# Kernel optimization log

Hardware: AMD Instinct MI355X
Metric: run time of the kernel (lower is better)

Reference implementation:

```python
import jax, jax.numpy as jnp
import numpy as np

def setup_inputs() -> dict:
    key = jax.random.key(0)
    k1, k2, k3, k4, k5 = jax.random.split(key, 5)
    B, Lc, Lq, D = 32, 512, 64, 1024
    return {
        "c": jax.random.normal(k1, (B, Lc, D), dtype=jnp.float32),
        "q": jax.random.normal(k2, (B, Lq, D), dtype=jnp.float32),
        "proj_c": jax.random.normal(k3, (D, 1), dtype=jnp.float32) * 0.04,
        "proj_q": jax.random.normal(k4, (D, 1), dtype=jnp.float32) * 0.04,
        "proj_cq": jax.random.normal(k5, (1, 1, D), dtype=jnp.float32) * 0.04,
    }

def reference(c, q, proj_c, proj_q, proj_cq):
    # similarity: s0 + s1 + s2, shape [B, Lc, Lq]
    s0 = c @ proj_c                                   # [B, Lc, 1]
    s1 = jnp.swapaxes(q @ proj_q, 1, 2)               # [B, 1, Lq]
    s2 = jnp.einsum('bcd,bqd->bcq', c * proj_cq, q)   # [B, Lc, Lq]
    sim = s0 + s1 + s2

    # context-to-query attention
    a_c2q = jax.nn.softmax(sim, axis=-1)              # [B, Lc, Lq]
    c2q = jnp.einsum('bcq,bqd->bcd', a_c2q, q)        # [B, Lc, D]

    # query-to-context attention (max over query dim, softmax over context)
    a_q2c = jax.nn.softmax(jnp.max(sim, axis=-1), axis=-1)  # [B, Lc]
    q2c = jnp.einsum('bc,bcd->bd', a_q2c, c)[:, None, :]    # [B, 1, D], broadcasts over Lc

    out = jnp.concatenate((c, c2q, c * q2c, c * c2q), axis=-1)  # [B, Lc, 4D]
    return out
```

## Files before the change

### kernel.cpp

```cpp
#include <hip/hip_runtime.h>

#define B 32
#define LC 512
#define LQ 64
#define DD 1024


typedef __attribute__((ext_vector_type(8))) short bf16x8;
typedef __attribute__((ext_vector_type(4))) float f32x4;

__device__ inline short f2bf(float f) {
    unsigned u = __builtin_bit_cast(unsigned, f);
    u += 0x7FFFu + ((u >> 16) & 1u);
    return (short)(u >> 16);
}

__device__ inline bf16x8 pack8(float4 a, float4 b) {
    bf16x8 r;
    r[0] = f2bf(a.x); r[1] = f2bf(a.y); r[2] = f2bf(a.z); r[3] = f2bf(a.w);
    r[4] = f2bf(b.x); r[5] = f2bf(b.y); r[6] = f2bf(b.z); r[7] = f2bf(b.w);
    return r;
}

__device__ inline float dot4(float4 a, float4 b) {
    return a.x * b.x + a.y * b.y + a.z * b.z + a.w * b.w;
}

__device__ inline int xswz(int bid, int nwg) {
    return (bid & 7) * (nwg >> 3) + (bid >> 3);
}

__device__ inline void xpose44(float v[4], int l15) {
    const bool m0 = l15 & 1, m1 = l15 & 2;
    float x0 = m0 ? v[0] : v[1];
    float x1 = m0 ? v[2] : v[3];
    x0 = __shfl_xor(x0, 1, 64);
    x1 = __shfl_xor(x1, 1, 64);
    if (m0) { v[0] = x0; v[2] = x1; } else { v[1] = x0; v[3] = x1; }
    float y0 = m1 ? v[0] : v[2];
    float y1 = m1 ? v[1] : v[3];
    y0 = __shfl_xor(y0, 2, 64);
    y1 = __shfl_xor(y1, 2, 64);
    if (m1) { v[0] = y0; v[1] = y1; } else { v[2] = y0; v[3] = y1; }
}

__global__ __launch_bounds__(256) void k0_q(const float* __restrict__ q,
                                            const float* __restrict__ proj_q,
                                            short* __restrict__ qbf,
                                            short* __restrict__ qT,
                                            float* __restrict__ s1part) {
    const int bid = xswz(blockIdx.x, 512);
    const int b  = bid >> 4;
    const int d0 = (bid & 15) * 64;
    const int sl = bid & 15;
    const int t  = threadIdx.x;

    __shared__ __align__(16) short tile[64][72];
    __shared__ float s1red[64][8];

    const int j0 = (t & 31) * 2;
    const int dg = t >> 5;

    const float* qr0 = q + (size_t)(b * LQ + j0) * DD + d0 + dg * 8;
    const float* qr1 = qr0 + DD;
    float4 x0 = *(const float4*)(qr0 + 0);
    float4 x1 = *(const float4*)(qr0 + 4);
    float4 y0 = *(const float4*)(qr1 + 0);
    float4 y1 = *(const float4*)(qr1 + 4);
    float4 p0 = *(const float4*)(proj_q + d0 + dg * 8);
    float4 p1 = *(const float4*)(proj_q + d0 + dg * 8 + 4);

    s1red[j0][dg]     = dot4(x0, p0) + dot4(x1, p1);
    s1red[j0 + 1][dg] = dot4(y0, p0) + dot4(y1, p1);

    *(bf16x8*)&qbf[(size_t)(b * LQ + j0) * DD + d0 + dg * 8]     = pack8(x0, x1);
    *(bf16x8*)&qbf[(size_t)(b * LQ + j0 + 1) * DD + d0 + dg * 8] = pack8(y0, y1);

    const float* fx0 = (const float*)&x0;
    const float* fx1 = (const float*)&x1;
    const float* fy0 = (const float*)&y0;
    const float* fy1 = (const float*)&y1;
#pragma unroll
    for (int e = 0; e < 8; ++e) {
        float v0 = (e < 4) ? fx0[e] : fx1[e - 4];
        float v1 = (e < 4) ? fy0[e] : fy1[e - 4];
        unsigned pk = (unsigned)(unsigned short)f2bf(v0)
                    | ((unsigned)(unsigned short)f2bf(v1) << 16);
        *(unsigned*)&tile[dg * 8 + e][j0] = pk;
    }
    __syncthreads();

    {
        const int d = t >> 2, part = t & 3;
        bf16x8 v0 = *(const bf16x8*)&tile[d][part * 16];
        bf16x8 v1 = *(const bf16x8*)&tile[d][part * 16 + 8];
        short* dst = qT + ((size_t)b * DD + d0 + d) * LQ + part * 16;
        *(bf16x8*)(dst)     = v0;
        *(bf16x8*)(dst + 8) = v1;
    }
    if (t < 64) {
        float s = 0.f;
#pragma unroll
        for (int k = 0; k < 8; ++k) s += s1red[t][k];
        s1part[(b * 16 + sl) * 64 + t] = s;
    }
}

__global__ __launch_bounds__(256) void k1_sim(const float* __restrict__ c,
                                              const short* __restrict__ qbf,
                                              const float* __restrict__ proj_c,
                                              const float* __restrict__ proj_cq,
                                              const float* __restrict__ s1part,
                                              short* __restrict__ P,
                                              float* __restrict__ mfull) {
    const int bid = xswz(blockIdx.x, 512);
    const int b  = bid >> 4;
    const int i0 = (bid & 15) * 32;
    const int t  = threadIdx.x;
    const int w  = t >> 6, lane = t & 63;
    const int l15 = lane & 15, quad = lane >> 4;

    __shared__ __align__(16) short sA[2][32][72];
    __shared__ float rmaxL[32][4];
    __shared__ float rsumL[32][4];
    __shared__ float s0red[32][8];
    __shared__ float s1L[64];

    const int arow = t >> 3, ag = t & 7;

    const float* cbase = c + (size_t)(b * LC + i0 + arow) * DD + ag * 8;
    const short* qfrag = qbf + (size_t)(b * LQ + w * 16 + l15) * DD + quad * 8;

    f32x4 acc[2] = {{0.f,0.f,0.f,0.f},{0.f,0.f,0.f,0.f}};
    float s0p = 0.f;

    float4 a0 = *(const float4*)(cbase + 0);
    float4 a1 = *(const float4*)(cbase + 4);
    bf16x8 bcur[2], bnxt[2];
#pragma unroll
    for (int s = 0; s < 2; ++s)
        bcur[s] = *(const bf16x8*)(qfrag + s * 32);
    {
        float4 p0 = *(const float4*)(proj_cq + ag * 8);
        float4 p1 = *(const float4*)(proj_cq + ag * 8 + 4);
        float4 c0 = *(const float4*)(proj_c + ag * 8);
        float4 c1 = *(const float4*)(proj_c + ag * 8 + 4);
        s0p += dot4(a0, c0) + dot4(a1, c1);
        float4 m0 = {a0.x * p0.x, a0.y * p0.y, a0.z * p0.z, a0.w * p0.w};
        float4 m1 = {a1.x * p1.x, a1.y * p1.y, a1.z * p1.z, a1.w * p1.w};
        *(bf16x8*)&sA[0][arow][ag * 8] = pack8(m0, m1);
    }
    a0 = *(const float4*)(cbase + 64);
    a1 = *(const float4*)(cbase + 68);
    __syncthreads();

    for (int kc = 0; kc < 16; ++kc) {
        const int cur = kc & 1;
        float4 na0, na1;
        if (kc < 14) {
            na0 = *(const float4*)(cbase + (kc + 2) * 64);
            na1 = *(const float4*)(cbase + (kc + 2) * 64 + 4);
        }
        if (kc < 15) {
#pragma unroll
            for (int s = 0; s < 2; ++s)
                bnxt[s] = *(const bf16x8*)(qfrag + (kc + 1) * 64 + s * 32);
        }
#pragma unroll
        for (int s = 0; s < 2; ++s) {
            int ko = s * 32 + quad * 8;
#pragma unroll
            for (int mt = 0; mt < 2; ++mt) {
                bf16x8 af = *(const bf16x8*)&sA[cur][mt * 16 + l15][ko];
                acc[mt] = __builtin_amdgcn_mfma_f32_16x16x32_bf16(af, bcur[s], acc[mt], 0, 0, 0);
            }
        }
        if (kc < 15) {
            const float* pcq = proj_cq + (kc + 1) * 64 + ag * 8;
            const float* pc  = proj_c  + (kc + 1) * 64 + ag * 8;
            float4 p0 = *(const float4*)(pcq + 0);
            float4 p1 = *(const float4*)(pcq + 4);
            float4 c0 = *(const float4*)(pc + 0);
            float4 c1 = *(const float4*)(pc + 4);
            s0p += dot4(a0, c0) + dot4(a1, c1);
            float4 m0 = {a0.x * p0.x, a0.y * p0.y, a0.z * p0.z, a0.w * p0.w};
            float4 m1 = {a1.x * p1.x, a1.y * p1.y, a1.z * p1.z, a1.w * p1.w};
            *(bf16x8*)&sA[cur ^ 1][arow][ag * 8] = pack8(m0, m1);
            a0 = na0; a1 = na1;
            bcur[0] = bnxt[0]; bcur[1] = bnxt[1];
        }
        __syncthreads();
    }

    s0red[arow][ag] = s0p;
    if (t < 64) {
        float s = 0.f;
#pragma unroll
        for (int k = 0; k < 16; ++k) s += s1part[(b * 16 + k) * 64 + t];
        s1L[t] = s;
    }
    __syncthreads();

    const float s1j = s1L[w * 16 + l15];
    float v[2][4];
#pragma unroll
    for (int mt = 0; mt < 2; ++mt) {
#pragma unroll
        for (int r = 0; r < 4; ++r) {
            float vv = acc[mt][r] + s1j;
            v[mt][r] = vv;
            float rm = vv;
#pragma unroll
            for (int off = 1; off < 16; off <<= 1) rm = fmaxf(rm, __shfl_xor(rm, off, 16));
            if (l15 == 0) rmaxL[mt * 16 + quad * 4 + r][w] = rm;
        }
    }
    __syncthreads();
    float e[2][4];
#pragma unroll
    for (int mt = 0; mt < 2; ++mt) {
#pragma unroll
        for (int r = 0; r < 4; ++r) {
            int row = mt * 16 + quad * 4 + r;
            float m = fmaxf(fmaxf(rmaxL[row][0], rmaxL[row][1]),
                            fmaxf(rmaxL[row][2], rmaxL[row][3]));
            float ee = __expf(v[mt][r] - m);
            e[mt][r] = ee;
            float se = ee;
#pragma unroll
            for (int off = 1; off < 16; off <<= 1) se += __shfl_xor(se, off, 16);
            if (l15 == 0) rsumL[row][w] = se;
        }
    }
    __syncthreads();
#pragma unroll
    for (int mt = 0; mt < 2; ++mt) {
#pragma unroll
        for (int r = 0; r < 4; ++r) {
            int row = mt * 16 + quad * 4 + r;
            float s = rsumL[row][0] + rsumL[row][1] + rsumL[row][2] + rsumL[row][3];
            P[(size_t)(b * LC + i0 + row) * LQ + w * 16 + l15] = f2bf(e[mt][r] / s);
        }
    }
    if (t < 32) {
        float s0v = 0.f;
#pragma unroll
        for (int k = 0; k < 8; ++k) s0v += s0red[t][k];
        float mm = fmaxf(fmaxf(rmaxL[t][0], rmaxL[t][1]),
                         fmaxf(rmaxL[t][2], rmaxL[t][3]));
        mfull[b * LC + i0 + t] = mm + s0v;
    }
}

__global__ __launch_bounds__(256) void k2_q2c(const float* __restrict__ c,
                                              const float* __restrict__ mfull,
                                              float* __restrict__ q2c) {
    const int bid = xswz(blockIdx.x, 256);
    const int b  = bid >> 3;
    const int d0 = (bid & 7) * 128;
    const int t  = threadIdx.x;
    __shared__ float aL[LC];
    __shared__ float redm[4];
    __shared__ float reds[4];

    float m0 = mfull[b * LC + t];
    float m1 = mfull[b * LC + 256 + t];
    float mx = fmaxf(m0, m1);
#pragma unroll
    for (int off = 32; off; off >>= 1) mx = fmaxf(mx, __shfl_xor(mx, off, 64));
    if ((t & 63) == 0) redm[t >> 6] = mx;
    __syncthreads();
    float bm = fmaxf(fmaxf(redm[0], redm[1]), fmaxf(redm[2], redm[3]));
    float e0 = __expf(m0 - bm), e1 = __expf(m1 - bm);
    float s = e0 + e1;
#pragma unroll
    for (int off = 32; off; off >>= 1) s += __shfl_xor(s, off, 64);
    if ((t & 63) == 0) reds[t >> 6] = s;
    __syncthreads();
    float bs = reds[0] + reds[1] + reds[2] + reds[3];
    float inv = 1.0f / bs;
    aL[t] = e0 * inv;
    aL[t + 256] = e1 * inv;
    __syncthreads();

    const int tx = t & 31, ty = t >> 5;
    float4 acc = {0.f, 0.f, 0.f, 0.f};
    const float* cb = c + (size_t)b * LC * DD + d0 + tx * 4;
    for (int i = ty; i < LC; i += 8) {
        float a = aL[i];
        float4 cv = *(const float4*)(cb + (size_t)i * DD);
        acc.x += a * cv.x; acc.y += a * cv.y; acc.z += a * cv.z; acc.w += a * cv.w;
    }
    __shared__ __align__(16) float4 red[8][32];
    red[ty][tx] = acc;
    __syncthreads();
    if (t < 32) {
        float4 sv = red[0][t];
#pragma unroll
        for (int k = 1; k < 8; ++k) {
            float4 v2 = red[k][t];
            sv.x += v2.x; sv.y += v2.y; sv.z += v2.z; sv.w += v2.w;
        }
        *(float4*)(q2c + b * DD + d0 + t * 4) = sv;
    }
}

__global__ __launch_bounds__(256) void k3_out(const float* __restrict__ c,
                                              const short* __restrict__ qT,
                                              const short* __restrict__ P,
                                              const float* __restrict__ q2c,
                                              float* __restrict__ out) {
    const int bid = xswz(blockIdx.x, 2048);
    const int b  = bid >> 6;
    const int i0 = ((bid >> 2) & 15) * 32;
    const int qd = bid & 3;
    const int t  = threadIdx.x;
    const int w  = t >> 6, lane = t & 63;
    const int l15 = lane & 15, quad = lane >> 4;

    bf16x8 paf[2][2];
#pragma unroll
    for (int s = 0; s < 2; ++s)
#pragma unroll
        for (int mt = 0; mt < 2; ++mt)
            paf[s][mt] = *(const bf16x8*)&P[(size_t)(b * LC + i0 + mt * 16 + l15) * LQ
                                           + s * 32 + quad * 8];

    const short* qTb = qT + ((size_t)b * DD + qd * 256 + w * 16 + l15) * LQ + quad * 8;

    for (int dci = 0; dci < 4; ++dci) {
        f32x4 acc2[2] = {{0.f,0.f,0.f,0.f},{0.f,0.f,0.f,0.f}};
#pragma unroll
        for (int s = 0; s < 2; ++s) {
            bf16x8 bf = *(const bf16x8*)(qTb + (size_t)dci * 64 * LQ + s * 32);
#pragma unroll
            for (int mt = 0; mt < 2; ++mt)
                acc2[mt] = __builtin_amdgcn_mfma_f32_16x16x32_bf16(paf[s][mt], bf, acc2[mt], 0, 0, 0);
        }

        float t0[4] = {acc2[0][0], acc2[0][1], acc2[0][2], acc2[0][3]};
        float t1[4] = {acc2[1][0], acc2[1][1], acc2[1][2], acc2[1][3]};
        xpose44(t0, l15);
        xpose44(t1, l15);

        const int dglob = qd * 256 + dci * 64 + w * 16 + 4 * (l15 >> 2);
        float4 g2 = *(const float4*)(q2c + b * DD + dglob);

#pragma unroll
        for (int mt = 0; mt < 2; ++mt) {
            const int row = i0 + mt * 16 + quad * 4 + (l15 & 3);
            float4 cqv = mt ? *(float4*)t1 : *(float4*)t0;
            float4 cc = *(const float4*)(c + (size_t)(b * LC + row) * DD + dglob);
            float* ob = out + (size_t)(b * LC + row) * (4 * DD) + dglob;
            *(float4*)(ob) = cc;
            *(float4*)(ob + DD) = cqv;
            float4 o2 = {cc.x * g2.x, cc.y * g2.y, cc.z * g2.z, cc.w * g2.w};
            *(float4*)(ob + 2 * DD) = o2;
            float4 o3 = {cc.x * cqv.x, cc.y * cqv.y, cc.z * cqv.z, cc.w * cqv.w};
            *(float4*)(ob + 3 * DD) = o3;
        }
    }
}

extern "C" void kernel_launch(void* const* d_in, const int* in_sizes, int n_in,
                              void* d_out, int out_size, void* d_ws, size_t ws_size,
                              hipStream_t stream) {
    const float* c       = (const float*)d_in[0];
    const float* q       = (const float*)d_in[1];
    const float* proj_c  = (const float*)d_in[2];
    const float* proj_q  = (const float*)d_in[3];
    const float* proj_cq = (const float*)d_in[4];
    float* out = (float*)d_out;
    float* ws  = (float*)d_ws;

    float* mfull  = ws;
    float* q2c    = ws + 16384;
    float* s1part = ws + 49152;
    short* P      = (short*)(ws + 81920);
    short* qbf    = (short*)(ws + 606208);
    short* qT     = (short*)(ws + 1654784);

    hipLaunchKernelGGL(k0_q,   dim3(512),  dim3(256), 0, stream, q, proj_q, qbf, qT, s1part);
    hipLaunchKernelGGL(k1_sim, dim3(512),  dim3(256), 0, stream,
                       c, qbf, proj_c, proj_cq, s1part, P, mfull);
    hipLaunchKernelGGL(k2_q2c, dim3(256),  dim3(256), 0, stream, c, mfull, q2c);
    hipLaunchKernelGGL(k3_out, dim3(2048), dim3(256), 0, stream, c, qT, P, q2c, out);
}
```

Measured before the change: 391.5 us.

## Move c*proj_cq bf16 conversion into prep kernel; stage full A tile in LDS

Adds a prep kernel that, in one half of its blocks, scales c by proj_cq, converts it to bf16 and computes s0, while the other half does the former q prep work. The similarity kernel then loads the whole 32x1024 bf16 A tile into LDS at once and runs the MFMA loop without the per-chunk double-buffer syncs. This cuts the fp32 c reads and ALU work inside k1. In exchange it adds a 32MB bf16 write and read through global memory and uses about 66KB of LDS per block, which may lower occupancy.

```diff
diff --git a/kernel.cpp b/kernel.cpp
--- a/kernel.cpp
+++ b/kernel.cpp
@@ -44,72 +44,109 @@
     if (m1) { v[0] = y0; v[1] = y1; } else { v[2] = y0; v[3] = y1; }
 }
 
-__global__ __launch_bounds__(256) void k0_q(const float* __restrict__ q,
-                                            const float* __restrict__ proj_q,
-                                            short* __restrict__ qbf,
-                                            short* __restrict__ qT,
-                                            float* __restrict__ s1part) {
-    const int bid = xswz(blockIdx.x, 512);
-    const int b  = bid >> 4;
-    const int d0 = (bid & 15) * 64;
-    const int sl = bid & 15;
-    const int t  = threadIdx.x;
-
-    __shared__ __align__(16) short tile[64][72];
-    __shared__ float s1red[64][8];
-
-    const int j0 = (t & 31) * 2;
-    const int dg = t >> 5;
-
-    const float* qr0 = q + (size_t)(b * LQ + j0) * DD + d0 + dg * 8;
-    const float* qr1 = qr0 + DD;
-    float4 x0 = *(const float4*)(qr0 + 0);
-    float4 x1 = *(const float4*)(qr0 + 4);
-    float4 y0 = *(const float4*)(qr1 + 0);
-    float4 y1 = *(const float4*)(qr1 + 4);
-    float4 p0 = *(const float4*)(proj_q + d0 + dg * 8);
-    float4 p1 = *(const float4*)(proj_q + d0 + dg * 8 + 4);
-
-    s1red[j0][dg]     = dot4(x0, p0) + dot4(x1, p1);
-    s1red[j0 + 1][dg] = dot4(y0, p0) + dot4(y1, p1);
-
-    *(bf16x8*)&qbf[(size_t)(b * LQ + j0) * DD + d0 + dg * 8]     = pack8(x0, x1);
-    *(bf16x8*)&qbf[(size_t)(b * LQ + j0 + 1) * DD + d0 + dg * 8] = pack8(y0, y1);
-
-    const float* fx0 = (const float*)&x0;
-    const float* fx1 = (const float*)&x1;
-    const float* fy0 = (const float*)&y0;
-    const float* fy1 = (const float*)&y1;
-#pragma unroll
-    for (int e = 0; e < 8; ++e) {
-        float v0 = (e < 4) ? fx0[e] : fx1[e - 4];
-        float v1 = (e < 4) ? fy0[e] : fy1[e - 4];
-        unsigned pk = (unsigned)(unsigned short)f2bf(v0)
-                    | ((unsigned)(unsigned short)f2bf(v1) << 16);
-        *(unsigned*)&tile[dg * 8 + e][j0] = pk;
-    }
-    __syncthreads();
-
-    {
-        const int d = t >> 2, part = t & 3;
-        bf16x8 v0 = *(const bf16x8*)&tile[d][part * 16];
-        bf16x8 v1 = *(const bf16x8*)&tile[d][part * 16 + 8];
-        short* dst = qT + ((size_t)b * DD + d0 + d) * LQ + part * 16;
-        *(bf16x8*)(dst)     = v0;
-        *(bf16x8*)(dst + 8) = v1;
-    }
-    if (t < 64) {
-        float s = 0.f;
-#pragma unroll
-        for (int k = 0; k < 8; ++k) s += s1red[t][k];
-        s1part[(b * 16 + sl) * 64 + t] = s;
-    }
-}
-
-__global__ __launch_bounds__(256) void k1_sim(const float* __restrict__ c,
+__global__ __launch_bounds__(256) void kprep(const float* __restrict__ c,
+                                             const float* __restrict__ q,
+                                             const float* __restrict__ proj_c,
+                                             const float* __restrict__ proj_q,
+                                             const float* __restrict__ proj_cq,
+                                             short* __restrict__ Abf,
+                                             float* __restrict__ s0g,
+                                             short* __restrict__ qbf,
+                                             short* __restrict__ qT,
+                                             float* __restrict__ s1part) {
+    const int half = blockIdx.x >> 9;
+    const int bid  = xswz(blockIdx.x & 511, 512);
+    const int t    = threadIdx.x;
+
+    if (half == 0) {
+        const int b  = bid >> 4;
+        const int i0 = (bid & 15) * 32;
+        const int arow = t >> 3, ag = t & 7;
+        __shared__ float s0red[32][8];
+
+        const float* cb = c + (size_t)(b * LC + i0 + arow) * DD + ag * 8;
+        short* ab = Abf + (size_t)(b * LC + i0 + arow) * DD + ag * 8;
+        float s0p = 0.f;
+#pragma unroll 4
+        for (int kc = 0; kc < 16; ++kc) {
+            float4 a0 = *(const float4*)(cb + kc * 64);
+            float4 a1 = *(const float4*)(cb + kc * 64 + 4);
+            float4 p0 = *(const float4*)(proj_cq + kc * 64 + ag * 8);
+            float4 p1 = *(const float4*)(proj_cq + kc * 64 + ag * 8 + 4);
+            float4 c0 = *(const float4*)(proj_c + kc * 64 + ag * 8);
+            float4 c1 = *(const float4*)(proj_c + kc * 64 + ag * 8 + 4);
+            s0p += dot4(a0, c0) + dot4(a1, c1);
+            float4 m0 = {a0.x * p0.x, a0.y * p0.y, a0.z * p0.z, a0.w * p0.w};
+            float4 m1 = {a1.x * p1.x, a1.y * p1.y, a1.z * p1.z, a1.w * p1.w};
+            *(bf16x8*)(ab + kc * 64) = pack8(m0, m1);
+        }
+        s0red[arow][ag] = s0p;
+        __syncthreads();
+        if (t < 32) {
+            float s = 0.f;
+#pragma unroll
+            for (int k = 0; k < 8; ++k) s += s0red[t][k];
+            s0g[b * LC + i0 + t] = s;
+        }
+    } else {
+        const int b  = bid >> 4;
+        const int d0 = (bid & 15) * 64;
+        const int sl = bid & 15;
+        __shared__ __align__(16) short tile[64][72];
+        __shared__ float s1red[64][8];
+
+        const int j0 = (t & 31) * 2;
+        const int dg = t >> 5;
+
+        const float* qr0 = q + (size_t)(b * LQ + j0) * DD + d0 + dg * 8;
+        const float* qr1 = qr0 + DD;
+        float4 x0 = *(const float4*)(qr0 + 0);
+        float4 x1 = *(const float4*)(qr0 + 4);
+        float4 y0 = *(const float4*)(qr1 + 0);
+        float4 y1 = *(const float4*)(qr1 + 4);
+        float4 p0 = *(const float4*)(proj_q + d0 + dg * 8);
+        float4 p1 = *(const float4*)(proj_q + d0 + dg * 8 + 4);
+
+        s1red[j0][dg]     = dot4(x0, p0) + dot4(x1, p1);
+        s1red[j0 + 1][dg] = dot4(y0, p0) + dot4(y1, p1);
+
+        *(bf16x8*)&qbf[(size_t)(b * LQ + j0) * DD + d0 + dg * 8]     = pack8(x0, x1);
+        *(bf16x8*)&qbf[(size_t)(b * LQ + j0 + 1) * DD + d0 + dg * 8] = pack8(y0, y1);
+
+        const float* fx0 = (const float*)&x0;
+        const float* fx1 = (const float*)&x1;
+        const float* fy0 = (const float*)&y0;
+        const float* fy1 = (const float*)&y1;
+#pragma unroll
+        for (int e = 0; e < 8; ++e) {
+            float v0 = (e < 4) ? fx0[e] : fx1[e - 4];
+            float v1 = (e < 4) ? fy0[e] : fy1[e - 4];
+            unsigned pk = (unsigned)(unsigned short)f2bf(v0)
+                        | ((unsigned)(unsigned short)f2bf(v1) << 16);
+            *(unsigned*)&tile[dg * 8 + e][j0] = pk;
+        }
+        __syncthreads();
+
+        {
+            const int d = t >> 2, part = t & 3;
+            bf16x8 v0 = *(const bf16x8*)&tile[d][part * 16];
+            bf16x8 v1 = *(const bf16x8*)&tile[d][part * 16 + 8];
+            short* dst = qT + ((size_t)b * DD + d0 + d) * LQ + part * 16;
+            *(bf16x8*)(dst)     = v0;
+            *(bf16x8*)(dst + 8) = v1;
+        }
+        if (t < 64) {
+            float s = 0.f;
+#pragma unroll
+            for (int k = 0; k < 8; ++k) s += s1red[t][k];
+            s1part[(b * 16 + sl) * 64 + t] = s;
+        }
+    }
+}
+
+__global__ __launch_bounds__(256) void k1_sim(const short* __restrict__ Abf,
                                               const short* __restrict__ qbf,
-                                              const float* __restrict__ proj_c,
-                                              const float* __restrict__ proj_cq,
+                                              const float* __restrict__ s0g,
                                               const float* __restrict__ s1part,
                                               short* __restrict__ P,
                                               float* __restrict__ mfull) {
@@ -120,79 +157,21 @@
     const int w  = t >> 6, lane = t & 63;
     const int l15 = lane & 15, quad = lane >> 4;
 
-    __shared__ __align__(16) short sA[2][32][72];
+    __shared__ __align__(16) short sA[32 * 1032];
     __shared__ float rmaxL[32][4];
     __shared__ float rsumL[32][4];
-    __shared__ float s0red[32][8];
     __shared__ float s1L[64];
 
     const int arow = t >> 3, ag = t & 7;
-
-    const float* cbase = c + (size_t)(b * LC + i0 + arow) * DD + ag * 8;
-    const short* qfrag = qbf + (size_t)(b * LQ + w * 16 + l15) * DD + quad * 8;
-
-    f32x4 acc[2] = {{0.f,0.f,0.f,0.f},{0.f,0.f,0.f,0.f}};
-    float s0p = 0.f;
-
-    float4 a0 = *(const float4*)(cbase + 0);
-    float4 a1 = *(const float4*)(cbase + 4);
-    bf16x8 bcur[2], bnxt[2];
-#pragma unroll
-    for (int s = 0; s < 2; ++s)
-        bcur[s] = *(const bf16x8*)(qfrag + s * 32);
-    {
-        float4 p0 = *(const float4*)(proj_cq + ag * 8);
-        float4 p1 = *(const float4*)(proj_cq + ag * 8 + 4);
-        float4 c0 = *(const float4*)(proj_c + ag * 8);
-        float4 c1 = *(const float4*)(proj_c + ag * 8 + 4);
-        s0p += dot4(a0, c0) + dot4(a1, c1);
-        float4 m0 = {a0.x * p0.x, a0.y * p0.y, a0.z * p0.z, a0.w * p0.w};
-        float4 m1 = {a1.x * p1.x, a1.y * p1.y, a1.z * p1.z, a1.w * p1.w};
-        *(bf16x8*)&sA[0][arow][ag * 8] = pack8(m0, m1);
-    }
-    a0 = *(const float4*)(cbase + 64);
-    a1 = *(const float4*)(cbase + 68);
-    __syncthreads();
-
-    for (int kc = 0; kc < 16; ++kc) {
-        const int cur = kc & 1;
-        float4 na0, na1;
-        if (kc < 14) {
-            na0 = *(const float4*)(cbase + (kc + 2) * 64);
-            na1 = *(const float4*)(cbase + (kc + 2) * 64 + 4);
-        }
-        if (kc < 15) {
-#pragma unroll
-            for (int s = 0; s < 2; ++s)
-                bnxt[s] = *(const bf16x8*)(qfrag + (kc + 1) * 64 + s * 32);
-        }
-#pragma unroll
-        for (int s = 0; s < 2; ++s) {
-            int ko = s * 32 + quad * 8;
-#pragma unroll
-            for (int mt = 0; mt < 2; ++mt) {
-                bf16x8 af = *(const bf16x8*)&sA[cur][mt * 16 + l15][ko];
-                acc[mt] = __builtin_amdgcn_mfma_f32_16x16x32_bf16(af, bcur[s], acc[mt], 0, 0, 0);
-            }
-        }
-        if (kc < 15) {
-            const float* pcq = proj_cq + (kc + 1) * 64 + ag * 8;
-            const float* pc  = proj_c  + (kc + 1) * 64 + ag * 8;
-            float4 p0 = *(const float4*)(pcq + 0);
-            float4 p1 = *(const float4*)(pcq + 4);
-            float4 c0 = *(const float4*)(pc + 0);
-            float4 c1 = *(const float4*)(pc + 4);
-            s0p += dot4(a0, c0) + dot4(a1, c1);
-            float4 m0 = {a0.x * p0.x, a0.y * p0.y, a0.z * p0.z, a0.w * p0.w};
-            float4 m1 = {a1.x * p1.x, a1.y * p1.y, a1.z * p1.z, a1.w * p1.w};
-            *(bf16x8*)&sA[cur ^ 1][arow][ag * 8] = pack8(m0, m1);
-            a0 = na0; a1 = na1;
-            bcur[0] = bnxt[0]; bcur[1] = bnxt[1];
-        }
-        __syncthreads();
-    }
-
-    s0red[arow][ag] = s0p;
+    const short* asrc = Abf + (size_t)(b * LC + i0 + arow) * DD + ag * 8;
+    short* adst = sA + arow * 1032 + ag * 8;
+
+    bf16x8 stg[16];
+#pragma unroll
+    for (int kc = 0; kc < 16; ++kc) stg[kc] = *(const bf16x8*)(asrc + kc * 64);
+#pragma unroll
+    for (int kc = 0; kc < 16; ++kc) *(bf16x8*)(adst + kc * 64) = stg[kc];
+
     if (t < 64) {
         float s = 0.f;
 #pragma unroll
@@ -200,6 +179,25 @@
         s1L[t] = s;
     }
     __syncthreads();
+
+    const short* qfrag = qbf + (size_t)(b * LQ + w * 16 + l15) * DD + quad * 8;
+    f32x4 acc[2] = {{0.f,0.f,0.f,0.f},{0.f,0.f,0.f,0.f}};
+
+#pragma unroll
+    for (int kc = 0; kc < 16; ++kc) {
+        bf16x8 bq0 = *(const bf16x8*)(qfrag + kc * 64);
+        bf16x8 bq1 = *(const bf16x8*)(qfrag + kc * 64 + 32);
+#pragma unroll
+        for (int mt = 0; mt < 2; ++mt) {
+            bf16x8 af = *(const bf16x8*)(sA + (mt * 16 + l15) * 1032 + kc * 64 + quad * 8);
+            acc[mt] = __builtin_amdgcn_mfma_f32_16x16x32_bf16(af, bq0, acc[mt], 0, 0, 0);
+        }
+#pragma unroll
+        for (int mt = 0; mt < 2; ++mt) {
+            bf16x8 af = *(const bf16x8*)(sA + (mt * 16 + l15) * 1032 + kc * 64 + 32 + quad * 8);
+            acc[mt] = __builtin_amdgcn_mfma_f32_16x16x32_bf16(af, bq1, acc[mt], 0, 0, 0);
+        }
+    }
 
     const float s1j = s1L[w * 16 + l15];
     float v[2][4];
@@ -243,12 +241,9 @@
         }
     }
     if (t < 32) {
-        float s0v = 0.f;
-#pragma unroll
-        for (int k = 0; k < 8; ++k) s0v += s0red[t][k];
         float mm = fmaxf(fmaxf(rmaxL[t][0], rmaxL[t][1]),
                          fmaxf(rmaxL[t][2], rmaxL[t][3]));
-        mfull[b * LC + i0 + t] = mm + s0v;
+        mfull[b * LC + i0 + t] = mm + s0g[b * LC + i0 + t];
     }
 }
 
@@ -374,15 +369,18 @@
     float* ws  = (float*)d_ws;
 
     float* mfull  = ws;
-    float* q2c    = ws + 16384;
-    float* s1part = ws + 49152;
-    short* P      = (short*)(ws + 81920);
-    short* qbf    = (short*)(ws + 606208);
-    short* qT     = (short*)(ws + 1654784);
-
-    hipLaunchKernelGGL(k0_q,   dim3(512),  dim3(256), 0, stream, q, proj_q, qbf, qT, s1part);
+    float* s0g    = ws + 16384;
+    float* q2c    = ws + 32768;
+    float* s1part = ws + 65536;
+    short* P      = (short*)(ws + 98304);
+    short* qbf    = (short*)(ws + 622592);
+    short* qT     = (short*)(ws + 1671168);
+    short* Abf    = (short*)(ws + 2719744);
+
+    hipLaunchKernelGGL(kprep, dim3(1024), dim3(256), 0, stream,
+                       c, q, proj_c, proj_q, proj_cq, Abf, s0g, qbf, qT, s1part);
     hipLaunchKernelGGL(k1_sim, dim3(512),  dim3(256), 0, stream,
-                       c, qbf, proj_c, proj_cq, s1part, P, mfull);
+                       Abf, qbf, s0g, s1part, P, mfull);
     hipLaunchKernelGGL(k2_q2c, dim3(256),  dim3(256), 0, stream, c, mfull, q2c);
     hipLaunchKernelGGL(k3_out, dim3(2048), dim3(256), 0, stream, c, qT, P, q2c, out);
 }
```

Result: slower. 417.1 us (+6.5%).
